# Optimization experiments

Measured on AMD Instinct MI355X. Metric: run time of the kernel, lower is better.

The kernel has to match this reference:

```python
import jax, jax.numpy as jnp
import numpy as np

B, S, D_MODEL = 2, 2048, 1024
HEADS = 16
DK = D_MODEL // HEADS  # 64
Q_RANK, RANK = 6, 2
ROPE_BASE = 10000.0


def _xavier(key, shape):
    # torch nn.init.xavier_uniform_ on weight (out,in); stored here as (in,out)
    fan_in, fan_out = shape
    a = (6.0 / (fan_in + fan_out)) ** 0.5
    return jax.random.uniform(key, shape, jnp.float32, -a, a)


def setup_inputs() -> dict:
    key = jax.random.key(0)
    ks = jax.random.split(key, 10)
    inp = {
        "q": jax.random.normal(ks[0], (B, S, D_MODEL), jnp.float32),
        "k": jax.random.normal(ks[1], (B, S, D_MODEL), jnp.float32),
        "v": jax.random.normal(ks[2], (B, S, D_MODEL), jnp.float32),
        # causal mask; mask==0 -> -inf in scores
        "mask": jnp.tril(jnp.ones((S, S), dtype=bool))[None, None],
        "W_Aq": _xavier(ks[3], (D_MODEL, Q_RANK * HEADS)),
        "W_Ak": _xavier(ks[4], (D_MODEL, RANK * HEADS)),
        "W_Av": _xavier(ks[5], (D_MODEL, RANK * HEADS)),
        "W_Bq": _xavier(ks[6], (D_MODEL, Q_RANK * DK)),
        "W_Bk": _xavier(ks[7], (D_MODEL, RANK * DK)),
        "W_Bv": _xavier(ks[8], (D_MODEL, RANK * DK)),
        "Wo": _xavier(ks[9], (D_MODEL, D_MODEL)),
    }
    return inp


def _rotary_cos_sin(seq_len, dim):
    inv_freq = 1.0 / (ROPE_BASE ** (jnp.arange(0, dim, 2, dtype=jnp.float32) / dim))
    freqs = jnp.outer(jnp.arange(seq_len, dtype=jnp.float32), inv_freq)  # [S, dim/2]
    return jnp.cos(freqs)[None, :, None, :], jnp.sin(freqs)[None, :, None, :]


def _apply_rotary(x, cos, sin):
    # x: [B, S, R, dk]; rotate-half style RoPE
    d = x.shape[-1] // 2
    x1, x2 = x[..., :d], x[..., d:]
    return jnp.concatenate([x1 * cos + x2 * sin, -x1 * sin + x2 * cos], axis=-1)


def reference(q, k, v, mask, W_Aq, W_Ak, W_Av, W_Bq, W_Bk, W_Bv, Wo):
    Bn, Sn, D = q.shape
    # low-rank factor projections
    A_q = (q @ W_Aq).reshape(Bn, Sn, HEADS, Q_RANK)
    A_k = (k @ W_Ak).reshape(Bn, Sn, HEADS, RANK)
    A_v = (v @ W_Av).reshape(Bn, Sn, HEADS, RANK)
    B_q = (q @ W_Bq).reshape(Bn, Sn, Q_RANK, DK)
    B_k = (k @ W_Bk).reshape(Bn, Sn, RANK, DK)
    B_v = (v @ W_Bv).reshape(Bn, Sn, RANK, DK)
    cos, sin = _rotary_cos_sin(Sn, DK)
    B_q = _apply_rotary(B_q, cos, sin)
    B_k = _apply_rotary(B_k, cos, sin)
    # reconstruct per-head q/k/v: [B,H,S,dk]
    qh = jnp.einsum("bshr,bsrd->bhsd", A_q, B_q) / Q_RANK
    kh = jnp.einsum("bshr,bsrd->bhsd", A_k, B_k) / RANK
    vh = jnp.einsum("bshr,bsrd->bhsd", A_v, B_v) / RANK
    # NOTE: original divides by d_k (not sqrt(d_k)) -- faithful to source
    score = jnp.einsum("bhqd,bhkd->bhqk", qh, kh) / DK
    score = jnp.where(mask, score, -jnp.inf)
    # dropout is identity (eval / dropout=0.0)
    att = jax.nn.softmax(score, axis=-1)
    out = jnp.einsum("bhqk,bhkd->bqhd", att, vh).reshape(Bn, Sn, D)
    return out @ Wo
```

## Files before the change

kernel.cpp:

```cpp
#include <hip/hip_runtime.h>
#include <hip/hip_bf16.h>


typedef __attribute__((ext_vector_type(8))) short short8;
typedef __attribute__((ext_vector_type(4))) float floatx4;

#define MFMA16(a, b, c) __builtin_amdgcn_mfma_f32_16x16x32_bf16(a, b, c, 0, 0, 0)

__device__ __forceinline__ float b2f(short s) {
    unsigned int u = ((unsigned int)(unsigned short)s) << 16;
    float f; __builtin_memcpy(&f, &u, 4); return f;
}
__device__ __forceinline__ unsigned short bfbits(float x) {
    __hip_bfloat16 h = __float2bfloat16(x);
    unsigned short u; __builtin_memcpy(&u, &h, 2); return u;
}

__device__ __forceinline__ float wsrc(int n, int k,
                                      const float* __restrict__ Aq, const float* __restrict__ Bq,
                                      const float* __restrict__ Ak, const float* __restrict__ Bk,
                                      const float* __restrict__ Av, const float* __restrict__ Bv,
                                      const float* __restrict__ Wo) {
    if (n < 96) return Aq[(size_t)k * 96 + n];
    if (n < 480) return Bq[(size_t)k * 384 + (n - 96)];
    if (n < 512) return 0.f;
    if (n < 544) return Ak[(size_t)k * 32 + (n - 512)];
    if (n < 672) return Bk[(size_t)k * 128 + (n - 544)];
    if (n < 768) return 0.f;
    if (n < 800) return Av[(size_t)k * 32 + (n - 768)];
    if (n < 928) return Bv[(size_t)k * 128 + (n - 800)];
    if (n < 1024) return 0.f;
    return Wo[(size_t)k * 1024 + (n - 1024)];
}

__global__ __launch_bounds__(256) void pack_wT_kernel(const float* __restrict__ Aq,
                                                      const float* __restrict__ Bq,
                                                      const float* __restrict__ Ak,
                                                      const float* __restrict__ Bk,
                                                      const float* __restrict__ Av,
                                                      const float* __restrict__ Bv,
                                                      const float* __restrict__ Wo,
                                                      __hip_bfloat16* __restrict__ outBase) {
    __shared__ float tile[64][65];
    int k0 = blockIdx.x * 64, n0 = blockIdx.y * 64;
    int tid = threadIdx.x;
#pragma unroll
    for (int p = 0; p < 16; ++p) {
        int idx = p * 256 + tid;
        int kl = idx >> 6, nl = idx & 63;
        tile[kl][nl] = wsrc(n0 + nl, k0 + kl, Aq, Bq, Ak, Bk, Av, Bv, Wo);
    }
    __syncthreads();
#pragma unroll
    for (int p = 0; p < 16; ++p) {
        int idx = p * 256 + tid;
        int nl = idx >> 6, kl = idx & 63;
        outBase[(size_t)(n0 + nl) * 1024 + k0 + kl] = __float2bfloat16(tile[kl][nl]);
    }
}

__global__ __launch_bounds__(256) void gemm3_kernel(const float* __restrict__ q,
                                                    const float* __restrict__ k,
                                                    const float* __restrict__ v,
                                                    const __hip_bfloat16* __restrict__ WT,
                                                    __hip_bfloat16* __restrict__ Pq,
                                                    __hip_bfloat16* __restrict__ Pk,
                                                    __hip_bfloat16* __restrict__ Pv) {
    __shared__ __align__(16) __hip_bfloat16 As[128][72];
    __shared__ __align__(16) __hip_bfloat16 Bs[128][72];
    int lin = blockIdx.x;
    int t = (lin >> 3) & 7;
    int m0 = ((lin & 7) + ((lin >> 6) << 3)) * 128;
    const float* A; __hip_bfloat16* C; int N, n0, wrow;
    if (t < 4)      { A = q; C = Pq; N = 512; n0 = t * 128;        wrow = t * 128; }
    else if (t < 6) { A = k; C = Pk; N = 256; n0 = (t - 4) * 128;  wrow = 512 + (t - 4) * 128; }
    else            { A = v; C = Pv; N = 256; n0 = (t - 6) * 128;  wrow = 768 + (t - 6) * 128; }
    int tid = threadIdx.x;
    int wave = tid >> 6, lane = tid & 63, quad = lane >> 4, l15 = lane & 15;
    int wm = wave >> 1, wn = wave & 1;
    floatx4 acc[4][4];
#pragma unroll
    for (int mt = 0; mt < 4; ++mt)
#pragma unroll
        for (int nt = 0; nt < 4; ++nt) acc[mt][nt] = (floatx4){0.f, 0.f, 0.f, 0.f};

    for (int k0 = 0; k0 < 1024; k0 += 64) {
#pragma unroll
        for (int pp = 0; pp < 8; ++pp) {
            int idx = pp * 256 + tid;
            int row = idx >> 4, c4 = (idx & 15) * 4;
            float4 av = *(const float4*)(A + (size_t)(m0 + row) * 1024 + k0 + c4);
            ushort4 bv;
            bv.x = bfbits(av.x); bv.y = bfbits(av.y); bv.z = bfbits(av.z); bv.w = bfbits(av.w);
            *(ushort4*)&As[row][c4] = bv;
        }
#pragma unroll
        for (int pp = 0; pp < 4; ++pp) {
            int idx = pp * 256 + tid;
            int row = idx >> 3, c8 = (idx & 7) * 8;
            *(uint4*)&Bs[row][c8] = *(const uint4*)(WT + (size_t)(wrow + row) * 1024 + k0 + c8);
        }
        __syncthreads();
#pragma unroll
        for (int ks = 0; ks < 64; ks += 32) {
            short8 af[4], bf[4];
#pragma unroll
            for (int t2 = 0; t2 < 4; ++t2) {
                af[t2] = *(const short8*)&As[wm * 64 + t2 * 16 + l15][ks + quad * 8];
                bf[t2] = *(const short8*)&Bs[wn * 64 + t2 * 16 + l15][ks + quad * 8];
            }
#pragma unroll
            for (int mt = 0; mt < 4; ++mt)
#pragma unroll
                for (int nt = 0; nt < 4; ++nt)
                    acc[mt][nt] = MFMA16(af[mt], bf[nt], acc[mt][nt]);
        }
        __syncthreads();
    }
#pragma unroll
    for (int mt = 0; mt < 4; ++mt)
#pragma unroll
        for (int nt = 0; nt < 4; ++nt)
#pragma unroll
            for (int r = 0; r < 4; ++r) {
                int row = m0 + wm * 64 + mt * 16 + quad * 4 + r;
                int col = n0 + wn * 64 + nt * 16 + l15;
                C[(size_t)row * N + col] = __float2bfloat16(acc[mt][nt][r]);
            }
}

__global__ __launch_bounds__(256) void gemm_out_kernel(const __hip_bfloat16* __restrict__ A,
                                                       const __hip_bfloat16* __restrict__ BT,
                                                       float* __restrict__ C) {
    __shared__ __align__(16) __hip_bfloat16 As[128][72];
    __shared__ __align__(16) __hip_bfloat16 Bs[128][72];
    int lin = blockIdx.x;
    int n0 = ((lin >> 3) & 7) * 128;
    int m0 = ((lin & 7) + ((lin >> 6) << 3)) * 128;
    int tid = threadIdx.x;
    int wave = tid >> 6, lane = tid & 63, quad = lane >> 4, l15 = lane & 15;
    int wm = wave >> 1, wn = wave & 1;
    floatx4 acc[4][4];
#pragma unroll
    for (int mt = 0; mt < 4; ++mt)
#pragma unroll
        for (int nt = 0; nt < 4; ++nt) acc[mt][nt] = (floatx4){0.f, 0.f, 0.f, 0.f};

    for (int k0 = 0; k0 < 1024; k0 += 64) {
#pragma unroll
        for (int pp = 0; pp < 4; ++pp) {
            int idx = pp * 256 + tid;
            int row = idx >> 3, c8 = (idx & 7) * 8;
            *(uint4*)&As[row][c8] = *(const uint4*)(A + (size_t)(m0 + row) * 1024 + k0 + c8);
            *(uint4*)&Bs[row][c8] = *(const uint4*)(BT + (size_t)(n0 + row) * 1024 + k0 + c8);
        }
        __syncthreads();
#pragma unroll
        for (int ks = 0; ks < 64; ks += 32) {
            short8 af[4], bf[4];
#pragma unroll
            for (int t2 = 0; t2 < 4; ++t2) {
                af[t2] = *(const short8*)&As[wm * 64 + t2 * 16 + l15][ks + quad * 8];
                bf[t2] = *(const short8*)&Bs[wn * 64 + t2 * 16 + l15][ks + quad * 8];
            }
#pragma unroll
            for (int mt = 0; mt < 4; ++mt)
#pragma unroll
                for (int nt = 0; nt < 4; ++nt)
                    acc[mt][nt] = MFMA16(af[mt], bf[nt], acc[mt][nt]);
        }
        __syncthreads();
    }
#pragma unroll
    for (int mt = 0; mt < 4; ++mt)
#pragma unroll
        for (int nt = 0; nt < 4; ++nt)
#pragma unroll
            for (int r = 0; r < 4; ++r) {
                int row = m0 + wm * 64 + mt * 16 + quad * 4 + r;
                int col = n0 + wn * 64 + nt * 16 + l15;
                C[(size_t)row * 1024 + col] = acc[mt][nt][r];
            }
}

__global__ __launch_bounds__(256) void combine_vt_kernel(const __hip_bfloat16* __restrict__ Pq,
                                                         const __hip_bfloat16* __restrict__ Pk,
                                                         const __hip_bfloat16* __restrict__ Pv,
                                                         __hip_bfloat16* __restrict__ qh,
                                                         __hip_bfloat16* __restrict__ kh,
                                                         __hip_bfloat16* __restrict__ vT) {
    __shared__ __align__(16) __hip_bfloat16 LAq[16][96];
    __shared__ __align__(16) __hip_bfloat16 LAk[16][32];
    __shared__ __align__(16) __hip_bfloat16 LAv[16][32];
    __shared__ __align__(16) __hip_bfloat16 LBq[16][6][72];
    __shared__ __align__(16) __hip_bfloat16 LBk[16][2][72];
    __shared__ __align__(16) __hip_bfloat16 LBv[16][2][72];
    int tid = threadIdx.x;
    int token0 = blockIdx.x * 16;
    int b = token0 >> 11, s0 = token0 & 2047, bh0 = b * 16;

    for (int i = tid; i < 16 * 512; i += 256) {
        int s = i >> 9, c = i & 511;
        __hip_bfloat16 val = Pq[(size_t)(token0 + s) * 512 + c];
        if (c < 96) LAq[s][c] = val;
        else if (c < 480) LBq[s][(c - 96) >> 6][(c - 96) & 63] = val;
    }
    for (int i = tid; i < 16 * 256; i += 256) {
        int s = i >> 8, c = i & 255;
        __hip_bfloat16 vk = Pk[(size_t)(token0 + s) * 256 + c];
        __hip_bfloat16 vv = Pv[(size_t)(token0 + s) * 256 + c];
        if (c < 32) { LAk[s][c] = vk; LAv[s][c] = vv; }
        else if (c < 160) {
            LBk[s][(c - 32) >> 6][(c - 32) & 63] = vk;
            LBv[s][(c - 32) >> 6][(c - 32) & 63] = vv;
        }
    }
    __syncthreads();
    for (int i = tid; i < 4096; i += 256) {
        int s = i >> 8, rr = (i >> 5) & 7, d = i & 31;
        float inv = __expf(-(float)d * 0.28782313662425576f);
        float rev = (float)(s0 + s) * inv * 0.15915494309189535f;
        rev -= floorf(rev);
        float sn = __builtin_amdgcn_sinf(rev);
        float cs = __builtin_amdgcn_cosf(rev);
        if (rr < 6) {
            float x1 = b2f(*(short*)&LBq[s][rr][d]), x2 = b2f(*(short*)&LBq[s][rr][d + 32]);
            LBq[s][rr][d] = __float2bfloat16(x1 * cs + x2 * sn);
            LBq[s][rr][d + 32] = __float2bfloat16(-x1 * sn + x2 * cs);
        } else {
            int r2 = rr - 6;
            float x1 = b2f(*(short*)&LBk[s][r2][d]), x2 = b2f(*(short*)&LBk[s][r2][d + 32]);
            LBk[s][r2][d] = __float2bfloat16(x1 * cs + x2 * sn);
            LBk[s][r2][d + 32] = __float2bfloat16(-x1 * sn + x2 * cs);
        }
    }
    __syncthreads();
    const float QSCALE = 1.4426950408889634f / 768.0f;
    {
        int s = tid >> 4, h = tid & 15;
        float aq[6], ak0, ak1;
#pragma unroll
        for (int r = 0; r < 6; ++r) aq[r] = b2f(*(short*)&LAq[s][h * 6 + r]);
        ak0 = b2f(*(short*)&LAk[s][h * 2]);
        ak1 = b2f(*(short*)&LAk[s][h * 2 + 1]);
        size_t obase = ((size_t)(bh0 + h) * 2048 + s0 + s) * 64;
#pragma unroll
        for (int dc = 0; dc < 64; dc += 8) {
            float accq[8] = {0, 0, 0, 0, 0, 0, 0, 0};
#pragma unroll
            for (int r = 0; r < 6; ++r) {
                short8 bq = *(const short8*)&LBq[s][r][dc];
#pragma unroll
                for (int e = 0; e < 8; ++e) accq[e] += aq[r] * b2f(bq[e]);
            }
            short8 bk0 = *(const short8*)&LBk[s][0][dc];
            short8 bk1 = *(const short8*)&LBk[s][1][dc];
            ushort outq[8], outk[8];
#pragma unroll
            for (int e = 0; e < 8; ++e) {
                outq[e] = bfbits(accq[e] * QSCALE);
                outk[e] = bfbits(ak0 * b2f(bk0[e]) + ak1 * b2f(bk1[e]));
            }
            *(uint4*)((__hip_bfloat16*)qh + obase + dc) = *(uint4*)outq;
            *(uint4*)((__hip_bfloat16*)kh + obase + dc) = *(uint4*)outk;
        }
    }
    {
        int s = tid & 15, dg = tid >> 4;
#pragma unroll
        for (int h = 0; h < 16; ++h) {
            float a0 = b2f(*(short*)&LAv[s][h * 2]) * 0.5f;
            float a1 = b2f(*(short*)&LAv[s][h * 2 + 1]) * 0.5f;
#pragma unroll
            for (int dd = 0; dd < 4; ++dd) {
                int d = dg * 4 + dd;
                float val = a0 * b2f(*(short*)&LBv[s][0][d]) + a1 * b2f(*(short*)&LBv[s][1][d]);
                vT[((size_t)(bh0 + h) * 64 + d) * 2048 + s0 + s] = __float2bfloat16(val);
            }
        }
    }
}

__global__ __launch_bounds__(256) void flash_kernel(const __hip_bfloat16* __restrict__ qh,
                                                    const __hip_bfloat16* __restrict__ kh,
                                                    const __hip_bfloat16* __restrict__ vT,
                                                    __hip_bfloat16* __restrict__ att) {
    int lin = blockIdx.x + (blockIdx.y << 5);
    int bh = ((lin & 7) << 2) | ((lin >> 3) & 3);
    int qi = 31 - (lin >> 5);
    int tid = threadIdx.x;
    int wave = tid >> 6, lane = tid & 63, quad = lane >> 4, l15 = lane & 15;
    int q0 = qi * 64;
    __shared__ __align__(16) __hip_bfloat16 Ks[64][72];
    __shared__ __align__(16) __hip_bfloat16 Vts[64][72];
    __shared__ __align__(16) __hip_bfloat16 Ps[4][16][72];

    const __hip_bfloat16* qrow = qh + ((size_t)bh * 2048 + q0 + wave * 16 + l15) * 64 + quad * 8;
    short8 aq0 = *(const short8*)(qrow);
    short8 aq1 = *(const short8*)(qrow + 32);

    floatx4 o[4];
#pragma unroll
    for (int nt = 0; nt < 4; ++nt) o[nt] = (floatx4){0.f, 0.f, 0.f, 0.f};
    float rs[4] = {0.f, 0.f, 0.f, 0.f};

    for (int j = 0; j <= qi; ++j) {
        int k0 = j * 64;
#pragma unroll
        for (int pp = 0; pp < 2; ++pp) {
            int idx = pp * 256 + tid;
            int row = idx >> 3, c8 = (idx & 7) * 8;
            *(uint4*)&Ks[row][c8] = *(const uint4*)(kh + ((size_t)bh * 2048 + k0 + row) * 64 + c8);
            *(uint4*)&Vts[row][c8] = *(const uint4*)(vT + ((size_t)bh * 64 + row) * 2048 + k0 + c8);
        }
        __syncthreads();

        floatx4 s[4];
#pragma unroll
        for (int nt = 0; nt < 4; ++nt) s[nt] = (floatx4){0.f, 0.f, 0.f, 0.f};
#pragma unroll
        for (int nt = 0; nt < 4; ++nt) {
            short8 bk0 = *(const short8*)&Ks[nt * 16 + l15][quad * 8];
            short8 bk1 = *(const short8*)&Ks[nt * 16 + l15][32 + quad * 8];
            s[nt] = MFMA16(aq0, bk0, s[nt]);
            s[nt] = MFMA16(aq1, bk1, s[nt]);
        }
        if (j == qi) {
            int rbase = wave * 16 + quad * 4;
#pragma unroll
            for (int nt = 0; nt < 4; ++nt) {
                int cl = nt * 16 + l15;
#pragma unroll
                for (int r = 0; r < 4; ++r)
                    if (cl > rbase + r) s[nt][r] = -__builtin_inff();
            }
        }
        float pv[4][4];
#pragma unroll
        for (int nt = 0; nt < 4; ++nt)
#pragma unroll
            for (int r = 0; r < 4; ++r) {
                pv[nt][r] = exp2f(s[nt][r]);
                rs[r] += pv[nt][r];
            }
#pragma unroll
        for (int nt = 0; nt < 4; ++nt)
#pragma unroll
            for (int r = 0; r < 4; ++r)
                Ps[wave][quad * 4 + r][nt * 16 + l15] = __float2bfloat16(pv[nt][r]);
        __builtin_amdgcn_s_waitcnt(0xC07F);
        short8 pa0 = *(const short8*)&Ps[wave][l15][quad * 8];
        short8 pa1 = *(const short8*)&Ps[wave][l15][32 + quad * 8];
#pragma unroll
        for (int nt = 0; nt < 4; ++nt) {
            short8 bv0 = *(const short8*)&Vts[nt * 16 + l15][quad * 8];
            short8 bv1 = *(const short8*)&Vts[nt * 16 + l15][32 + quad * 8];
            o[nt] = MFMA16(pa0, bv0, o[nt]);
            o[nt] = MFMA16(pa1, bv1, o[nt]);
        }
        __syncthreads();
    }
    float l_i[4];
#pragma unroll
    for (int r = 0; r < 4; ++r) {
        float x = rs[r];
        x += __shfl_xor(x, 1, 64);
        x += __shfl_xor(x, 2, 64);
        x += __shfl_xor(x, 4, 64);
        x += __shfl_xor(x, 8, 64);
        l_i[r] = x;
    }
    int b = bh >> 4, h = bh & 15;
    size_t obase = ((size_t)b * 2048 + q0 + wave * 16 + quad * 4) * 1024 + h * 64;
#pragma unroll
    for (int nt = 0; nt < 4; ++nt)
#pragma unroll
        for (int r = 0; r < 4; ++r)
            att[obase + (size_t)r * 1024 + nt * 16 + l15] = __float2bfloat16(o[nt][r] / l_i[r]);
}

extern "C" void kernel_launch(void* const* d_in, const int* in_sizes, int n_in,
                              void* d_out, int out_size, void* d_ws, size_t ws_size,
                              hipStream_t stream) {
    const float* q = (const float*)d_in[0];
    const float* k = (const float*)d_in[1];
    const float* v = (const float*)d_in[2];
    const float* W_Aq = (const float*)d_in[4];
    const float* W_Ak = (const float*)d_in[5];
    const float* W_Av = (const float*)d_in[6];
    const float* W_Bq = (const float*)d_in[7];
    const float* W_Bk = (const float*)d_in[8];
    const float* W_Bv = (const float*)d_in[9];
    const float* Wo = (const float*)d_in[10];
    float* out = (float*)d_out;

    char* w = (char*)d_ws;
    __hip_bfloat16* qh  = (__hip_bfloat16*)(w + 0);
    __hip_bfloat16* kh  = (__hip_bfloat16*)(w + 8388608);
    __hip_bfloat16* vT  = (__hip_bfloat16*)(w + 16777216);
    __hip_bfloat16* WT  = (__hip_bfloat16*)(w + 25165824);
    __hip_bfloat16* WoT = WT + (size_t)1024 * 1024;
    __hip_bfloat16* Pq  = (__hip_bfloat16*)(w + 29360128);
    __hip_bfloat16* Pk  = (__hip_bfloat16*)(w + 33554432);
    __hip_bfloat16* Pv  = (__hip_bfloat16*)(w + 35651584);
    __hip_bfloat16* att = (__hip_bfloat16*)(w + 37748736);

    pack_wT_kernel<<<dim3(16, 32), 256, 0, stream>>>(W_Aq, W_Bq, W_Ak, W_Bk, W_Av, W_Bv, Wo, WT);
    gemm3_kernel<<<256, 256, 0, stream>>>(q, k, v, WT, Pq, Pk, Pv);
    combine_vt_kernel<<<256, 256, 0, stream>>>(Pq, Pk, Pv, qh, kh, vT);
    flash_kernel<<<dim3(32, 32), 256, 0, stream>>>(qh, kh, vT, att);
    gemm_out_kernel<<<256, 256, 0, stream>>>(att, WoT, out);
}
```

Before: 259.9 us.

## Compute transposed S tile so P feeds PV MFMA from registers without LDS

```diff
diff --git a/kernel.cpp b/kernel.cpp
--- a/kernel.cpp
+++ b/kernel.cpp
@@ -293,7 +293,6 @@
     int q0 = qi * 64;
     __shared__ __align__(16) __hip_bfloat16 Ks[64][72];
     __shared__ __align__(16) __hip_bfloat16 Vts[64][72];
-    __shared__ __align__(16) __hip_bfloat16 Ps[4][16][72];
 
     const __hip_bfloat16* qrow = qh + ((size_t)bh * 2048 + q0 + wave * 16 + l15) * 64 + quad * 8;
     short8 aq0 = *(const short8*)(qrow);
@@ -302,7 +301,8 @@
     floatx4 o[4];
 #pragma unroll
     for (int nt = 0; nt < 4; ++nt) o[nt] = (floatx4){0.f, 0.f, 0.f, 0.f};
-    float rs[4] = {0.f, 0.f, 0.f, 0.f};
+    float rs = 0.f;
+    int qloc = wave * 16 + l15;
 
     for (int j = 0; j <= qi; ++j) {
         int k0 = j * 64;
@@ -322,17 +322,16 @@
         for (int nt = 0; nt < 4; ++nt) {
             short8 bk0 = *(const short8*)&Ks[nt * 16 + l15][quad * 8];
             short8 bk1 = *(const short8*)&Ks[nt * 16 + l15][32 + quad * 8];
-            s[nt] = MFMA16(aq0, bk0, s[nt]);
-            s[nt] = MFMA16(aq1, bk1, s[nt]);
+            s[nt] = MFMA16(bk0, aq0, s[nt]);
+            s[nt] = MFMA16(bk1, aq1, s[nt]);
         }
         if (j == qi) {
-            int rbase = wave * 16 + quad * 4;
 #pragma unroll
             for (int nt = 0; nt < 4; ++nt) {
-                int cl = nt * 16 + l15;
+                int kbase = nt * 16 + quad * 4;
 #pragma unroll
                 for (int r = 0; r < 4; ++r)
-                    if (cl > rbase + r) s[nt][r] = -__builtin_inff();
+                    if (kbase + r > qloc) s[nt][r] = -__builtin_inff();
             }
         }
         float pv[4][4];
@@ -341,42 +340,41 @@
 #pragma unroll
             for (int r = 0; r < 4; ++r) {
                 pv[nt][r] = exp2f(s[nt][r]);
-                rs[r] += pv[nt][r];
-            }
-#pragma unroll
-        for (int nt = 0; nt < 4; ++nt)
-#pragma unroll
-            for (int r = 0; r < 4; ++r)
-                Ps[wave][quad * 4 + r][nt * 16 + l15] = __float2bfloat16(pv[nt][r]);
-        __builtin_amdgcn_s_waitcnt(0xC07F);
-        short8 pa0 = *(const short8*)&Ps[wave][l15][quad * 8];
-        short8 pa1 = *(const short8*)&Ps[wave][l15][32 + quad * 8];
+                rs += pv[nt][r];
+            }
+        union { ushort u[8]; short8 v; } p0, p1;
+#pragma unroll
+        for (int r = 0; r < 4; ++r) {
+            p0.u[r]     = bfbits(pv[0][r]);
+            p0.u[4 + r] = bfbits(pv[1][r]);
+            p1.u[r]     = bfbits(pv[2][r]);
+            p1.u[4 + r] = bfbits(pv[3][r]);
+        }
 #pragma unroll
         for (int nt = 0; nt < 4; ++nt) {
-            short8 bv0 = *(const short8*)&Vts[nt * 16 + l15][quad * 8];
-            short8 bv1 = *(const short8*)&Vts[nt * 16 + l15][32 + quad * 8];
-            o[nt] = MFMA16(pa0, bv0, o[nt]);
-            o[nt] = MFMA16(pa1, bv1, o[nt]);
-        }
-        __syncthreads();
-    }
-    float l_i[4];
-#pragma unroll
-    for (int r = 0; r < 4; ++r) {
-        float x = rs[r];
-        x += __shfl_xor(x, 1, 64);
-        x += __shfl_xor(x, 2, 64);
-        x += __shfl_xor(x, 4, 64);
-        x += __shfl_xor(x, 8, 64);
-        l_i[r] = x;
-    }
+            int vr = nt * 16 + l15;
+            union { ushort4 h[2]; short8 v; } x0, x1;
+            x0.h[0] = *(const ushort4*)&Vts[vr][quad * 4];
+            x0.h[1] = *(const ushort4*)&Vts[vr][16 + quad * 4];
+            x1.h[0] = *(const ushort4*)&Vts[vr][32 + quad * 4];
+            x1.h[1] = *(const ushort4*)&Vts[vr][48 + quad * 4];
+            o[nt] = MFMA16(x0.v, p0.v, o[nt]);
+            o[nt] = MFMA16(x1.v, p1.v, o[nt]);
+        }
+        __syncthreads();
+    }
+    rs += __shfl_xor(rs, 16, 64);
+    rs += __shfl_xor(rs, 32, 64);
+    float inv = 1.0f / rs;
     int b = bh >> 4, h = bh & 15;
-    size_t obase = ((size_t)b * 2048 + q0 + wave * 16 + quad * 4) * 1024 + h * 64;
-#pragma unroll
-    for (int nt = 0; nt < 4; ++nt)
-#pragma unroll
-        for (int r = 0; r < 4; ++r)
-            att[obase + (size_t)r * 1024 + nt * 16 + l15] = __float2bfloat16(o[nt][r] / l_i[r]);
+    size_t obase = ((size_t)b * 2048 + q0 + wave * 16 + l15) * 1024 + h * 64 + quad * 4;
+#pragma unroll
+    for (int nt = 0; nt < 4; ++nt) {
+        ushort ow[4];
+#pragma unroll
+        for (int r = 0; r < 4; ++r) ow[r] = bfbits(o[nt][r] * inv);
+        *(ushort4*)((__hip_bfloat16*)att + obase + nt * 16) = *(ushort4*)ow;
+    }
 }
 
 extern "C" void kernel_launch(void* const* d_in, const int* in_sizes, int n_in,
```

Result: no change. 258.7 us (-0.5%).
